# Kernel optimization log

Hardware: AMD Instinct MI355X
Metric: run time of the kernel (lower is better)

The kernel has to match this reference:

```python
import jax, jax.numpy as jnp
import numpy as np

HID = 2048      # hidden_size
NH = 32         # num query heads
NKV = 8         # num kv heads
HD = HID // NH  # head_dim = 64
E = 4           # num_experts
N = 2048        # flattened token count (divisible by E)
THETA = 10000.0
EPS = 1e-6


def setup_inputs() -> dict:
    key = jax.random.key(0)
    ks = jax.random.split(key, 8)
    s = HID ** -0.5
    return {
        "hidden_states": jax.random.normal(ks[0], (N, HID), jnp.float32),
        "positions": jnp.arange(N, dtype=jnp.int32),
        "sort_idx": jax.random.permutation(ks[1], N).astype(jnp.int32),
        "q_proj_w": jax.random.normal(ks[2], (E, HID, NH * HD), jnp.float32) * s,
        "o_proj_w": jax.random.normal(ks[3], (E, NH * HD, HID), jnp.float32) * s,
        "k_w": jax.random.normal(ks[4], (HID, NKV * HD), jnp.float32) * s,
        "v_w": jax.random.normal(ks[5], (HID, NKV * HD), jnp.float32) * s,
        "q_norm_w": jnp.ones((HD,), jnp.float32),
        "k_norm_w": jnp.ones((HD,), jnp.float32),
    }


def _routed_proj(x, weight, sort_idx):
    # x: [N, din], weight: [E, din, dout], sort_idx: permutation of N
    n, din = x.shape
    e, _, dout = weight.shape
    chunk = n // e
    sorted_x = x[sort_idx].reshape(e, chunk, din)          # gather + split
    sorted_out = jnp.einsum('ecd,edo->eco', sorted_x, weight).reshape(n, dout)
    return jnp.zeros((n, dout), sorted_out.dtype).at[sort_idx].set(sorted_out)


def _rms_norm(x, w):
    # x: [N, H, D] normalized over last dim
    var = jnp.mean(jnp.square(x), axis=-1, keepdims=True)
    return x * jax.lax.rsqrt(var + EPS) * w


def _rope_neox(x, positions):
    # x: [N, H, D]
    half = HD // 2
    inv_freq = 1.0 / (THETA ** (jnp.arange(0, HD, 2, dtype=jnp.float32) / HD))  # [D/2]
    freqs = positions.astype(jnp.float32)[:, None] * inv_freq                   # [N, D/2]
    cos = jnp.cos(freqs)[:, None, :]  # [N,1,D/2]
    sin = jnp.sin(freqs)[:, None, :]
    x1, x2 = x[..., :half], x[..., half:]
    return jnp.concatenate([x1 * cos - x2 * sin, x2 * cos + x1 * sin], axis=-1)


def reference(hidden_states, positions, sort_idx, q_proj_w, o_proj_w, k_w, v_w,
              q_norm_w, k_norm_w):
    n = hidden_states.shape[0]
    # projections
    q = _routed_proj(hidden_states, q_proj_w, sort_idx)        # [N, NH*HD]
    k = hidden_states @ k_w                                    # [N, NKV*HD]
    v = hidden_states @ v_w                                    # [N, NKV*HD]
    # qk norm per head
    q = _rms_norm(q.reshape(n, NH, HD), q_norm_w)
    k = _rms_norm(k.reshape(n, NKV, HD), k_norm_w)
    # rotary (neox style)
    q = _rope_neox(q, positions)
    k = _rope_neox(k, positions)
    v = v.reshape(n, NKV, HD)
    # GQA causal attention over the packed sequence
    g = NH // NKV
    k_rep = jnp.repeat(k, g, axis=1)  # [N, NH, HD]
    v_rep = jnp.repeat(v, g, axis=1)
    scores = jnp.einsum('qhd,khd->hqk', q, k_rep) * (HD ** -0.5)
    causal = positions[:, None] >= positions[None, :]          # [N, N]
    scores = jnp.where(causal[None], scores, jnp.finfo(scores.dtype).min)
    attn = jax.nn.softmax(scores, axis=-1)
    o = jnp.einsum('hqk,khd->qhd', attn, v_rep).reshape(n, NH * HD)
    # routed output projection
    return _routed_proj(o, o_proj_w, sort_idx)
```

## Files before the change

### kernel.cpp

```cpp
#include <hip/hip_runtime.h>
#include <hip/hip_bf16.h>

#define N_TOK 2048
#define HID   2048
#define NH    32
#define NKV   8
#define HD    64
#define NEXP  4
#define CHUNK (N_TOK / NEXP)

typedef __attribute__((ext_vector_type(8))) short short8;
typedef __attribute__((ext_vector_type(4))) short short4v;
typedef __attribute__((ext_vector_type(4))) float float4v;

#define QSCALE (0.125f * 1.44269504f)
#define RLOG   0.41524101186f

__device__ inline short f2bf(float f) {
    __hip_bfloat16 h = __float2bfloat16(f);
    return *reinterpret_cast<short*>(&h);
}
__device__ inline float bf2f(short s) {
    __hip_bfloat16 h = *reinterpret_cast<__hip_bfloat16*>(&s);
    return __bfloat162float(h);
}
__device__ __forceinline__ float fast_exp2(float x) {
    float r;
    asm("v_exp_f32 %0, %1" : "=v"(r) : "v"(x));
    return r;
}

__device__ __forceinline__ void gld_lds16(const void* g, void* l) {
    __builtin_amdgcn_global_load_lds(
        (const __attribute__((address_space(1))) unsigned int*)g,
        (__attribute__((address_space(3))) unsigned int*)l, 16, 0, 0);
}

__device__ __forceinline__ void wtrans_tile(
    const float* __restrict__ in, short* __restrict__ out, int Nw,
    int k0, int n0, float (*T)[65], int t)
{
#pragma unroll
    for (int i = 0; i < 16; i++) {
        int idx = t + i * 256, kl = idx >> 6, nl = idx & 63;
        T[kl][nl] = in[(size_t)(k0 + kl) * Nw + n0 + nl];
    }
    __syncthreads();
#pragma unroll
    for (int i = 0; i < 2; i++) {
        int idx = t + i * 256;
        int nl = idx >> 3, k8 = (idx & 7) * 8;
        short8 s;
#pragma unroll
        for (int j = 0; j < 8; j++) s[j] = f2bf(T[k8 + j][nl]);
        *(short8*)&out[(size_t)(n0 + nl) * 2048 + k0 + k8] = s;
    }
}

__global__ __launch_bounds__(256)
void prep1(const float* __restrict__ hidden, const float* __restrict__ qw,
           const float* __restrict__ kw, const float* __restrict__ vw,
           short* __restrict__ Xbf, short* __restrict__ Wq,
           short* __restrict__ Wkv)
{
    __shared__ float T[64][65];
    const int b = blockIdx.x;
    const int t = threadIdx.x;

    if (b < 2048) {
        size_t i = (size_t)b * 256 + t;
        float4 a = ((const float4*)hidden)[i * 2];
        float4 c = ((const float4*)hidden)[i * 2 + 1];
        short8 s;
        s[0] = f2bf(a.x); s[1] = f2bf(a.y); s[2] = f2bf(a.z); s[3] = f2bf(a.w);
        s[4] = f2bf(c.x); s[5] = f2bf(c.y); s[6] = f2bf(c.z); s[7] = f2bf(c.w);
        ((short8*)Xbf)[i] = s;
    } else if (b < 6144) {
        int b2 = b - 2048;
        int k0 = (b2 & 31) * 64, n0 = ((b2 >> 5) & 31) * 64, e = b2 >> 10;
        wtrans_tile(qw + (size_t)e * 2048 * 2048, Wq + (size_t)e * 2048 * 2048,
                    2048, k0, n0, T, t);
    } else {
        int b3 = b - 6144;
        int k0 = (b3 & 31) * 64, n0 = ((b3 >> 5) & 7) * 64, z = b3 >> 8;
        wtrans_tile(z ? vw : kw, Wkv + (size_t)z * 512 * 2048, 512, k0, n0, T, t);
    }
}

template <int EPI>
__device__ __forceinline__ void gemm_core(
    const short* __restrict__ X, const short* __restrict__ Wt,
    const int* __restrict__ sidx, void* __restrict__ OUT,
    int dout, bool routed, int bx, int by,
    const int* __restrict__ positions, const float* __restrict__ nw,
    short* __restrict__ vt,
    short* As0, short* Bs0, short* As1, short* Bs1, int* ridx)
{
    const int t  = threadIdx.x;
    const int m0 = by * 128;
    const int n0 = bx * 128;

    if (t < 128) ridx[t] = routed ? sidx[m0 + t] : (m0 + t);
    __syncthreads();

    const short* Wb = Wt + (routed ? (size_t)(m0 / CHUNK) * (size_t)dout * 2048 : 0);

    const int seg = (t & 3) * 8;
    const short* ga0 = X  + (size_t)ridx[t >> 2] * 2048 + seg;
    const short* ga1 = X  + (size_t)ridx[64 + (t >> 2)] * 2048 + seg;
    const short* gb0 = Wb + (size_t)(n0 + (t >> 2)) * 2048 + seg;
    const short* gb1 = Wb + (size_t)(n0 + 64 + (t >> 2)) * 2048 + seg;

    const int lane = t & 63;
    const int wave = t >> 6;
    const int wl   = wave * 64 * 8;
    const int col  = lane & 15;
    const int rowg = lane >> 4;
    const int wm   = (wave >> 1) * 64;
    const int wn   = (wave & 1) * 64;

    int offA[4], offB[4];
#pragma unroll
    for (int i = 0; i < 4; i++) {
        offA[i] = (wm + i * 16 + col) * 32 + rowg * 8;
        offB[i] = (wn + i * 16 + col) * 32 + rowg * 8;
    }

    float4v acc[4][4];
#pragma unroll
    for (int mt = 0; mt < 4; mt++)
#pragma unroll
        for (int nt = 0; nt < 4; nt++) acc[mt][nt] = (float4v){0.f, 0.f, 0.f, 0.f};

    auto stage = [&](int k0, short* A, short* B) {
        gld_lds16(ga0 + k0, A + wl);
        gld_lds16(ga1 + k0, A + 256 * 8 + wl);
        gld_lds16(gb0 + k0, B + wl);
        gld_lds16(gb1 + k0, B + 256 * 8 + wl);
    };
    auto compute = [&](const short* A, const short* B) {
        short8 af[4], bfr[4];
#pragma unroll
        for (int i = 0; i < 4; i++) af[i] = *(const short8*)&A[offA[i]];
#pragma unroll
        for (int i = 0; i < 4; i++) bfr[i] = *(const short8*)&B[offB[i]];
#pragma unroll
        for (int mt = 0; mt < 4; mt++)
#pragma unroll
            for (int nt = 0; nt < 4; nt++)
                acc[mt][nt] = __builtin_amdgcn_mfma_f32_16x16x32_bf16(
                    af[mt], bfr[nt], acc[mt][nt], 0, 0, 0);
    };

    stage(0, As0, Bs0);
    asm volatile("s_waitcnt vmcnt(0)" ::: "memory");
    __builtin_amdgcn_s_barrier();

    for (int k0 = 0; k0 < 2048; k0 += 64) {
        stage(k0 + 32, As1, Bs1);
        compute(As0, Bs0);
        asm volatile("s_waitcnt vmcnt(0)" ::: "memory");
        __builtin_amdgcn_s_barrier();

        if (k0 + 64 < 2048) stage(k0 + 64, As0, Bs0);
        compute(As1, Bs1);
        asm volatile("s_waitcnt vmcnt(0)" ::: "memory");
        __builtin_amdgcn_s_barrier();
    }

    if (EPI == 0) {
#pragma unroll
        for (int mt = 0; mt < 4; mt++)
#pragma unroll
            for (int r = 0; r < 4; r++) {
                int row = ridx[wm + mt * 16 + rowg * 4 + r];
#pragma unroll
                for (int nt = 0; nt < 4; nt++)
                    ((float*)OUT)[(size_t)row * dout + n0 + wn + nt * 16 + col] =
                        acc[mt][nt][r];
            }
        return;
    }

    const bool is_v = (EPI == 2) && (n0 + wn >= 512);

    if (is_v) {
#pragma unroll
        for (int mt = 0; mt < 4; mt++) {
            int rowb = m0 + wm + mt * 16 + rowg * 4;
#pragma unroll
            for (int nt = 0; nt < 4; nt++) {
                int d = n0 + wn + nt * 16 + col - 512;
                short4v sv;
#pragma unroll
                for (int r = 0; r < 4; r++) sv[r] = f2bf(acc[mt][nt][r]);
                *(short4v*)&vt[(size_t)d * N_TOK + rowb] = sv;
            }
        }
        return;
    }

    {
        const int   h     = (n0 + wn) >> 6;
        const float oscl  = (EPI == 1) ? QSCALE : 1.0f;
        const int   ldo   = (EPI == 1) ? 2048 : 512;
        short* ob = (short*)OUT;
        float invf0 = fast_exp2(-(float)col * RLOG);
        float invf1 = fast_exp2(-(float)(16 + col) * RLOG);
        float wv[4];
#pragma unroll
        for (int nt = 0; nt < 4; nt++) wv[nt] = nw[nt * 16 + col];

#pragma unroll
        for (int mt = 0; mt < 4; mt++)
#pragma unroll
            for (int r = 0; r < 4; r++) {
                int row = ridx[wm + mt * 16 + rowg * 4 + r];
                float x0 = acc[mt][0][r], x1 = acc[mt][1][r];
                float x2 = acc[mt][2][r], x3 = acc[mt][3][r];
                float ss = x0 * x0 + x1 * x1 + x2 * x2 + x3 * x3;
#pragma unroll
                for (int off = 1; off < 16; off <<= 1)
                    ss += __shfl_xor(ss, off, 64);
                float rs = rsqrtf(ss * (1.0f / HD) + 1e-6f);
                x0 *= rs * wv[0]; x1 *= rs * wv[1];
                x2 *= rs * wv[2]; x3 *= rs * wv[3];
                float pos = (float)positions[row];
                float fr0 = pos * invf0, fr1 = pos * invf1;
                float c0 = __cosf(fr0), s0 = __sinf(fr0);
                float c1 = __cosf(fr1), s1 = __sinf(fr1);
                float o0 = x0 * c0 - x2 * s0;
                float o1 = x1 * c1 - x3 * s1;
                float o2 = x2 * c0 + x0 * s0;
                float o3 = x3 * c1 + x1 * s1;
                size_t base = (size_t)row * ldo + h * 64 + col;
                ob[base]      = f2bf(o0 * oscl);
                ob[base + 16] = f2bf(o1 * oscl);
                ob[base + 32] = f2bf(o2 * oscl);
                ob[base + 48] = f2bf(o3 * oscl);
            }
    }
}

__global__ __launch_bounds__(256)
void gemm_qkv(const short* __restrict__ X, const short* __restrict__ Wq,
              const short* __restrict__ Wkv, const int* __restrict__ sidx,
              short* __restrict__ qb, short* __restrict__ kb,
              short* __restrict__ vt, const int* __restrict__ positions,
              const float* __restrict__ qnw, const float* __restrict__ knw)
{
    __shared__ __align__(16) short As0[128 * 32], Bs0[128 * 32];
    __shared__ __align__(16) short As1[128 * 32], Bs1[128 * 32];
    __shared__ int ridx[128];
    int b = blockIdx.x;
    if (b < 256)
        gemm_core<1>(X, Wq, sidx, qb, 2048, true, b & 15, b >> 4,
                     positions, qnw, nullptr, As0, Bs0, As1, Bs1, ridx);
    else {
        b -= 256;
        gemm_core<2>(X, Wkv, nullptr, kb, 1024, false, b & 7, b >> 3,
                     positions, knw, vt, As0, Bs0, As1, Bs1, ridx);
    }
}

__global__ __launch_bounds__(256)
void gemm_o(const short* __restrict__ X, const short* __restrict__ Wt,
            const int* __restrict__ sidx, float* __restrict__ OUT)
{
    __shared__ __align__(16) short As0[128 * 32], Bs0[128 * 32];
    __shared__ __align__(16) short As1[128 * 32], Bs1[128 * 32];
    __shared__ int ridx[128];
    gemm_core<0>(X, Wt, sidx, OUT, 2048, true, blockIdx.x, blockIdx.y,
                 nullptr, nullptr, nullptr, As0, Bs0, As1, Bs1, ridx);
}

__global__ __launch_bounds__(256)
void attn_plus(const short* __restrict__ qb, const short* __restrict__ kb,
               const short* __restrict__ vt, const int* __restrict__ positions,
               short* __restrict__ ob,
               const float* __restrict__ ow, short* __restrict__ Wo)
{
    __shared__ __align__(16) char smem[27648];
    const int b = blockIdx.x;
    const int t = threadIdx.x;

    if (b >= 512) {
        float (*T)[65] = (float(*)[65])smem;
        int b2 = b - 512;
        int k0 = (b2 & 31) * 64, n0 = ((b2 >> 5) & 31) * 64, e = b2 >> 10;
        wtrans_tile(ow + (size_t)e * 2048 * 2048, Wo + (size_t)e * 2048 * 2048,
                    2048, k0, n0, T, t);
        return;
    }

    short (*Ks)[72] = (short(*)[72])smem;
    short (*Vt)[72] = (short(*)[72])(smem + 64 * 72 * 2);
    short (*Ps)[72] = (short(*)[72])(smem + 2 * 64 * 72 * 2);

    const int head = b >> 4;
    const int kvh  = head >> 2;
    const int lane = t & 63;
    const int wave = t >> 6;
    const int rowg = lane >> 4;
    const int col  = lane & 15;

    const int sr = t >> 2;
    const int sc = (t & 3) * 16;
    const float BIAS = 9.0f * 1.44269504f;

#pragma unroll
    for (int pass = 0; pass < 2; pass++) {
        const int qt = pass == 0 ? (31 - (b & 15)) : (b & 15);
        const int q0 = qt * 64;
        const int m0 = q0 + wave * 16;

        const short* qrow = qb + (size_t)(m0 + col) * HID + head * HD;
        short8 aq0 = *(const short8*)(qrow + rowg * 8);
        short8 aq1 = *(const short8*)(qrow + 32 + rowg * 8);

        int pq[4];
        float l_i[4];
#pragma unroll
        for (int r = 0; r < 4; r++) {
            pq[r] = positions[m0 + rowg * 4 + r];
            l_i[r] = 0.f;
        }
        float4v oacc[4];
#pragma unroll
        for (int n = 0; n < 4; n++) oacc[n] = (float4v){0.f, 0.f, 0.f, 0.f};

        const short* kpb = kb + (size_t)sr * 512 + kvh * HD + sc;
        const short* vpb = vt + ((size_t)kvh * HD + sr) * N_TOK + sc;

        const int nkt = qt + 1;
        short8 kA, kB, vA, vB;
        {
            kA = *(const short8*)(kpb);
            kB = *(const short8*)(kpb + 8);
            vA = *(const short8*)(vpb);
            vB = *(const short8*)(vpb + 8);
        }

        for (int kt = 0; kt < nkt; kt++) {
            __syncthreads();
            *(short8*)&Ks[sr][sc]     = kA;
            *(short8*)&Ks[sr][sc + 8] = kB;
            *(short8*)&Vt[sr][sc]     = vA;
            *(short8*)&Vt[sr][sc + 8] = vB;
            __syncthreads();

            if (kt + 1 < nkt) {
                kA = *(const short8*)(kpb + (size_t)(kt + 1) * 64 * 512);
                kB = *(const short8*)(kpb + (size_t)(kt + 1) * 64 * 512 + 8);
                vA = *(const short8*)(vpb + (kt + 1) * 64);
                vB = *(const short8*)(vpb + (kt + 1) * 64 + 8);
            }

            const int k0 = kt * 64;
            float4v c[4];
#pragma unroll
            for (int j = 0; j < 4; j++) {
                short8 blo = *(const short8*)&Ks[j * 16 + col][rowg * 8];
                short8 bhi = *(const short8*)&Ks[j * 16 + col][32 + rowg * 8];
                float4v cc = (float4v){0.f, 0.f, 0.f, 0.f};
                cc = __builtin_amdgcn_mfma_f32_16x16x32_bf16(aq0, blo, cc, 0, 0, 0);
                cc = __builtin_amdgcn_mfma_f32_16x16x32_bf16(aq1, bhi, cc, 0, 0, 0);
                c[j] = cc;
            }

            if (kt == qt) {
#pragma unroll
                for (int j = 0; j < 4; j++) {
                    int pk = positions[k0 + j * 16 + col];
#pragma unroll
                    for (int r = 0; r < 4; r++)
                        if (pq[r] < pk) c[j][r] = -1e30f;
                }
            }

#pragma unroll
            for (int j = 0; j < 4; j++)
#pragma unroll
                for (int r = 0; r < 4; r++) {
                    float p = fast_exp2(c[j][r] - BIAS);
                    l_i[r] += p;
                    Ps[wave * 16 + rowg * 4 + r][j * 16 + col] = f2bf(p);
                }

            __asm__ volatile("s_waitcnt lgkmcnt(0)" ::: "memory");

            short8 ap0 = *(const short8*)&Ps[wave * 16 + col][rowg * 8];
            short8 ap1 = *(const short8*)&Ps[wave * 16 + col][32 + rowg * 8];
#pragma unroll
            for (int n = 0; n < 4; n++) {
                short8 blo = *(const short8*)&Vt[n * 16 + col][rowg * 8];
                short8 bhi = *(const short8*)&Vt[n * 16 + col][32 + rowg * 8];
                float4v a2 = oacc[n];
                a2 = __builtin_amdgcn_mfma_f32_16x16x32_bf16(ap0, blo, a2, 0, 0, 0);
                a2 = __builtin_amdgcn_mfma_f32_16x16x32_bf16(ap1, bhi, a2, 0, 0, 0);
                oacc[n] = a2;
            }
        }

#pragma unroll
        for (int r = 0; r < 4; r++) {
#pragma unroll
            for (int off = 1; off < 16; off <<= 1)
                l_i[r] += __shfl_xor(l_i[r], off, 64);
            l_i[r] = 1.f / l_i[r];
        }
#pragma unroll
        for (int n = 0; n < 4; n++)
#pragma unroll
            for (int r = 0; r < 4; r++)
                ob[(size_t)(m0 + rowg * 4 + r) * HID + head * HD + n * 16 + col] =
                    f2bf(oacc[n][r] * l_i[r]);
    }
}

extern "C" void kernel_launch(void* const* d_in, const int* in_sizes, int n_in,
                              void* d_out, int out_size, void* d_ws, size_t ws_size,
                              hipStream_t stream)
{
    (void)in_sizes; (void)n_in; (void)out_size; (void)ws_size;

    const float* hidden    = (const float*)d_in[0];
    const int*   positions = (const int*)  d_in[1];
    const int*   sort_idx  = (const int*)  d_in[2];
    const float* q_proj_w  = (const float*)d_in[3];
    const float* o_proj_w  = (const float*)d_in[4];
    const float* k_w       = (const float*)d_in[5];
    const float* v_w       = (const float*)d_in[6];
    const float* q_norm_w  = (const float*)d_in[7];
    const float* k_norm_w  = (const float*)d_in[8];
    float* out = (float*)d_out;

    const size_t M1 = 1024 * 1024;
    short* Wqo = (short*)d_ws;
    short* Wkv = Wqo + 16 * M1;
    short* Xbf = Wkv + 2 * M1;
    short* qb  = Xbf + 4 * M1;
    short* kb  = qb  + 4 * M1;
    short* vt  = kb  + 1 * M1;
    short* obf = Xbf;

    prep1<<<6656, 256, 0, stream>>>(hidden, q_proj_w, k_w, v_w, Xbf, Wqo, Wkv);

    gemm_qkv<<<384, 256, 0, stream>>>(Xbf, Wqo, Wkv, sort_idx, qb, kb, vt,
                                      positions, q_norm_w, k_norm_w);

    attn_plus<<<4608, 256, 0, stream>>>(qb, kb, vt, positions, obf,
                                        o_proj_w, Wqo);

    gemm_o<<<dim3(16, 16), 256, 0, stream>>>(obf, Wqo, sort_idx, out);
}
```

Measured before the change: 301.4 us.

## Triple-buffer GEMM LDS pipeline, swizzle LDS layout, vectorize weight transpose loads

The GEMM main loop moves from a two-stage to a three-stage LDS ring with partial vmcnt waits, so two K-slices of global loads stay in flight while the current slice is computed. The LDS write location and the fragment read offsets are XOR-swizzled together to cut bank conflicts on the short8 fragment reads. The weight transpose tile now reads float4 vectors instead of scalar floats. The extra LDS buffers raise shared memory per block by half, which may lower occupancy.

```diff
diff --git a/kernel.cpp b/kernel.cpp
--- a/kernel.cpp
+++ b/kernel.cpp
@@ -40,10 +40,13 @@
     const float* __restrict__ in, short* __restrict__ out, int Nw,
     int k0, int n0, float (*T)[65], int t)
 {
-#pragma unroll
-    for (int i = 0; i < 16; i++) {
-        int idx = t + i * 256, kl = idx >> 6, nl = idx & 63;
-        T[kl][nl] = in[(size_t)(k0 + kl) * Nw + n0 + nl];
+    const int nl4 = (t & 15) * 4;
+    const int kl  = t >> 4;
+#pragma unroll
+    for (int i = 0; i < 4; i++) {
+        float4 v = *(const float4*)&in[(size_t)(k0 + kl + i * 16) * Nw + n0 + nl4];
+        float* Tr = &T[kl + i * 16][nl4];
+        Tr[0] = v.x; Tr[1] = v.y; Tr[2] = v.z; Tr[3] = v.w;
     }
     __syncthreads();
 #pragma unroll
@@ -94,7 +97,8 @@
     int dout, bool routed, int bx, int by,
     const int* __restrict__ positions, const float* __restrict__ nw,
     short* __restrict__ vt,
-    short* As0, short* Bs0, short* As1, short* Bs1, int* ridx)
+    short* As0, short* Bs0, short* As1, short* Bs1,
+    short* As2, short* Bs2, int* ridx)
 {
     const int t  = threadIdx.x;
     const int m0 = by * 128;
@@ -105,7 +109,7 @@
 
     const short* Wb = Wt + (routed ? (size_t)(m0 / CHUNK) * (size_t)dout * 2048 : 0);
 
-    const int seg = (t & 3) * 8;
+    const int seg = (((t & 3) ^ ((t >> 3) & 3))) * 8;
     const short* ga0 = X  + (size_t)ridx[t >> 2] * 2048 + seg;
     const short* ga1 = X  + (size_t)ridx[64 + (t >> 2)] * 2048 + seg;
     const short* gb0 = Wb + (size_t)(n0 + (t >> 2)) * 2048 + seg;
@@ -119,11 +123,12 @@
     const int wm   = (wave >> 1) * 64;
     const int wn   = (wave & 1) * 64;
 
+    const int swz = (col >> 1) & 3;
     int offA[4], offB[4];
 #pragma unroll
     for (int i = 0; i < 4; i++) {
-        offA[i] = (wm + i * 16 + col) * 32 + rowg * 8;
-        offB[i] = (wn + i * 16 + col) * 32 + rowg * 8;
+        offA[i] = (wm + i * 16 + col) * 32 + ((rowg ^ swz) * 8);
+        offB[i] = (wn + i * 16 + col) * 32 + ((rowg ^ swz) * 8);
     }
 
     float4v acc[4][4];
@@ -153,19 +158,27 @@
     };
 
     stage(0, As0, Bs0);
-    asm volatile("s_waitcnt vmcnt(0)" ::: "memory");
+    stage(32, As1, Bs1);
+    asm volatile("s_waitcnt vmcnt(4)" ::: "memory");
     __builtin_amdgcn_s_barrier();
 
-    for (int k0 = 0; k0 < 2048; k0 += 64) {
-        stage(k0 + 32, As1, Bs1);
-        compute(As0, Bs0);
-        asm volatile("s_waitcnt vmcnt(0)" ::: "memory");
+    short *Ac = As0, *Bc = Bs0;
+    short *An = As1, *Bn = Bs1;
+    short *Af = As2, *Bf = Bs2;
+#pragma unroll 1
+    for (int k0 = 0; k0 < 2048; k0 += 32) {
+        if (k0 + 64 < 2048) {
+            stage(k0 + 64, Af, Bf);
+            compute(Ac, Bc);
+            asm volatile("s_waitcnt vmcnt(4)" ::: "memory");
+        } else {
+            compute(Ac, Bc);
+            asm volatile("s_waitcnt vmcnt(0)" ::: "memory");
+        }
         __builtin_amdgcn_s_barrier();
-
-        if (k0 + 64 < 2048) stage(k0 + 64, As0, Bs0);
-        compute(As1, Bs1);
-        asm volatile("s_waitcnt vmcnt(0)" ::: "memory");
-        __builtin_amdgcn_s_barrier();
+        short* tp;
+        tp = Ac; Ac = An; An = Af; Af = tp;
+        tp = Bc; Bc = Bn; Bn = Bf; Bf = tp;
     }
 
     if (EPI == 0) {
@@ -251,15 +264,16 @@
 {
     __shared__ __align__(16) short As0[128 * 32], Bs0[128 * 32];
     __shared__ __align__(16) short As1[128 * 32], Bs1[128 * 32];
+    __shared__ __align__(16) short As2[128 * 32], Bs2[128 * 32];
     __shared__ int ridx[128];
     int b = blockIdx.x;
     if (b < 256)
         gemm_core<1>(X, Wq, sidx, qb, 2048, true, b & 15, b >> 4,
-                     positions, qnw, nullptr, As0, Bs0, As1, Bs1, ridx);
+                     positions, qnw, nullptr, As0, Bs0, As1, Bs1, As2, Bs2, ridx);
     else {
         b -= 256;
         gemm_core<2>(X, Wkv, nullptr, kb, 1024, false, b & 7, b >> 3,
-                     positions, knw, vt, As0, Bs0, As1, Bs1, ridx);
+                     positions, knw, vt, As0, Bs0, As1, Bs1, As2, Bs2, ridx);
     }
 }
 
@@ -269,9 +283,10 @@
 {
     __shared__ __align__(16) short As0[128 * 32], Bs0[128 * 32];
     __shared__ __align__(16) short As1[128 * 32], Bs1[128 * 32];
+    __shared__ __align__(16) short As2[128 * 32], Bs2[128 * 32];
     __shared__ int ridx[128];
     gemm_core<0>(X, Wt, sidx, OUT, 2048, true, blockIdx.x, blockIdx.y,
-                 nullptr, nullptr, nullptr, As0, Bs0, As1, Bs1, ridx);
+                 nullptr, nullptr, nullptr, As0, Bs0, As1, Bs1, As2, Bs2, ridx);
 }
 
 __global__ __launch_bounds__(256)
```

Measured after the change: 327.6 us. +8.7%, slower.
